# Kernel optimization log

Hardware: AMD Instinct MI355X
Metric: run time of the kernel (lower is better)

## Reference

```python
import math
import jax, jax.numpy as jnp
import numpy as np

B, T, D_MODEL, H = 8, 2048, 1024, 16
D_HEAD = D_MODEL // H


def _rel_shift(x):
    # x: (B, T, H, H) -- faithful port of the TF pad/reshape/slice trick,
    # which in this module operates on the time axis (dim 1).
    b, t, h, h2 = x.shape
    x = jnp.pad(x, ((0, 0), (1, 0), (0, 0), (0, 0)))  # (B, T+1, H, H)
    x = x.reshape(t + 1, b, h, h2)[1:]                 # drop first row
    return x.reshape(b, t, h, h2)


def setup_inputs() -> dict:
    key = jax.random.key(0)
    ks = jax.random.split(key, 16)
    s = 1.0 / math.sqrt(D_MODEL)
    return {
        "inputs": jax.random.normal(ks[0], (B, T, D_MODEL), jnp.float32),
        "pos_embedding": jax.random.normal(ks[1], (B, T, D_MODEL), jnp.float32),
        "masks": jnp.ones((B, T), dtype=bool),
        "Wq": jax.random.normal(ks[2], (D_MODEL, D_MODEL), jnp.float32) * s,
        "bq": jnp.zeros((D_MODEL,), jnp.float32),
        "Wk": jax.random.normal(ks[3], (D_MODEL, D_MODEL), jnp.float32) * s,
        "bk": jnp.zeros((D_MODEL,), jnp.float32),
        "Wv": jax.random.normal(ks[4], (D_MODEL, D_MODEL), jnp.float32) * s,
        "bv": jnp.zeros((D_MODEL,), jnp.float32),
        "Wp": jax.random.normal(ks[5], (D_MODEL, D_MODEL), jnp.float32) * s,
        "Wo": jax.random.normal(ks[6], (D_MODEL, D_MODEL), jnp.float32) * s,
        "bo": jnp.zeros((D_MODEL,), jnp.float32),
        "u_bias": jax.random.normal(ks[7], (H, D_HEAD), jnp.float32) * 0.05,
        "v_bias": jax.random.normal(ks[8], (H, D_HEAD), jnp.float32) * 0.05,
    }


def reference(inputs, pos_embedding, masks, Wq, bq, Wk, bk, Wv, bv, Wp, Wo, bo, u_bias, v_bias):
    b, t, _ = inputs.shape
    sqrt_dim = math.sqrt(D_MODEL)
    q = (inputs @ Wq + bq).reshape(b, t, H, D_HEAD)
    k = (inputs @ Wk + bk).reshape(b, t, H, D_HEAD)
    v = (inputs @ Wv + bv).reshape(b, t, H, D_HEAD)
    p = (pos_embedding @ Wp).reshape(b, t, H, D_HEAD)

    # NOTE: no (B,H,T,D) transpose in the original -> HxH scores per timestep.
    content_score = jnp.einsum("bthd,btkd->bthk", q + u_bias, k)  # (B,T,H,H)
    pos_score = jnp.einsum("bthd,btkd->bthk", q + v_bias, p)      # (B,T,H,H)
    pos_score = _rel_shift(pos_score)
    score = (content_score + pos_score) / sqrt_dim
    score = jnp.where(masks[:, :, None, None], score, jnp.float32(1e-9))
    attn = jax.nn.softmax(score, axis=-1)
    ctx = jnp.einsum("bthk,btkd->bthd", attn, v)                  # (B,T,H,D)
    ctx = ctx.transpose(0, 2, 1, 3).reshape(b, -1, D_MODEL)       # (B,T,d_model)
    return ctx @ Wo + bo
```

## Files before the change

### kernel.cpp

```cpp
#include <hip/hip_runtime.h>


typedef __attribute__((ext_vector_type(8))) short short8;
typedef __attribute__((ext_vector_type(4))) float f32x4;

__device__ __forceinline__ ushort f2bf(float f) {
    unsigned u = __float_as_uint(f);
    u += 0x7FFFu + ((u >> 16) & 1u);
    return (ushort)(u >> 16);
}
__device__ __forceinline__ float bf2f(ushort u) {
    return __uint_as_float(((unsigned)u) << 16);
}

typedef const unsigned int __attribute__((address_space(1)))* gas_t;
typedef unsigned int __attribute__((address_space(3)))* las_t;
__device__ __forceinline__ void gl_lds16(const ushort* g, ushort* l) {
    __builtin_amdgcn_global_load_lds((gas_t)g, (las_t)l, 16, 0, 0);
}

__global__ __launch_bounds__(256)
void conv_bf16_k(const float* __restrict__ in, ushort* __restrict__ out)
{
    const size_t i = ((size_t)blockIdx.x * 256 + threadIdx.x) * 8;
    float4 a = *(const float4*)(in + i);
    float4 b = *(const float4*)(in + i + 4);
    short8 o = {(short)f2bf(a.x), (short)f2bf(a.y), (short)f2bf(a.z), (short)f2bf(a.w),
                (short)f2bf(b.x), (short)f2bf(b.y), (short)f2bf(b.z), (short)f2bf(b.w)};
    *(short8*)(out + i) = o;
}

__global__ __launch_bounds__(256)
void transpose5_k(const float* __restrict__ W0, const float* __restrict__ W1,
                  const float* __restrict__ W2, const float* __restrict__ W3,
                  const float* __restrict__ W4, ushort* __restrict__ Wt)
{
    __shared__ float tile[32][33];
    const int z = blockIdx.z;
    const float* W = (z == 0) ? W0 : (z == 1) ? W1 : (z == 2) ? W2 : (z == 3) ? W3 : W4;
    ushort* dst = Wt + (size_t)z * 1024 * 1024;
    const int tx = threadIdx.x & 31;
    const int ty = threadIdx.x >> 5;
    const int n0 = blockIdx.x * 32;
    const int k0 = blockIdx.y * 32;
#pragma unroll
    for (int i = 0; i < 4; ++i)
        tile[ty + i * 8][tx] = W[(size_t)(k0 + ty + i * 8) * 1024 + n0 + tx];
    __syncthreads();
#pragma unroll
    for (int i = 0; i < 4; ++i)
        dst[(size_t)(n0 + ty + i * 8) * 1024 + k0 + tx] = f2bf(tile[tx][ty + i * 8]);
}

__global__ __launch_bounds__(256)
void bias_concat_k(const float* __restrict__ b0, const float* __restrict__ b1,
                   const float* __restrict__ b2, float* __restrict__ out)
{
    const int i = blockIdx.x * 256 + threadIdx.x;
    const int s = i >> 10;
    const int j = i & 1023;
    out[i] = (s == 0) ? b0[j] : (s == 1) ? b1[j] : b2[j];
}


#define VMC(n) asm volatile("s_waitcnt vmcnt(" #n ")" ::: "memory")
#define KDIM 1024

template<int HAS_BIAS, int OUT_BF16>
__global__ __launch_bounds__(512, 2)
void gemm9_k(const ushort* __restrict__ A, const ushort* __restrict__ Bt,
             const float* __restrict__ bias, void* __restrict__ Cv,
             int N)
{
    __shared__ ushort As[3 * 4096];
    __shared__ ushort Bs[3 * 8192];
    const int tid = threadIdx.x;
    const int l = tid & 63;
    const int w = tid >> 6;
    const int wr = w >> 2;
    const int wc = w & 3;

    const int gx = gridDim.x;
    const int lin = blockIdx.y * gx + blockIdx.x;
    const int xcd = lin & 7;
    const int idx = lin >> 3;
    const int hb = gridDim.y >> 3;
    const int sxc = gx >> 2;
    const int g4 = idx >> 4;
    const int li = idx & 15;
    const int bx = (g4 % sxc) * 4 + (li & 3);
    const int by = xcd * hb + (g4 / sxc) * 4 + (li >> 2);
    const int bm = by * 128;
    const int bn = bx * 256;

    const int srow = tid >> 2;
    const int scol = ((tid & 3) ^ ((tid >> 3) & 3)) * 8;
    const ushort* Ag  = A  + (size_t)(bm + srow) * KDIM + scol;
    const ushort* Bg  = Bt + (size_t)(bn + srow) * KDIM + scol;
    const ushort* Bg2 = Bg + (size_t)128 * KDIM;
    const int lw = w * 512;

    const int lr = l & 15;
    const int fb = (((l >> 4) ^ ((l >> 1) & 3)) * 8);
    const int laneA = (wr * 64 + lr) * 32 + fb;
    const int laneB = (wc * 64 + lr) * 32 + fb;

    f32x4 acc[4][4];
#pragma unroll
    for (int i = 0; i < 4; ++i)
#pragma unroll
        for (int n = 0; n < 4; ++n)
            acc[i][n] = (f32x4){0.f, 0.f, 0.f, 0.f};

    short8 fa[2][4], fbv[2][4];

#define STAGE9(tt, rg) do { \
    ushort* ha = As + (rg) * 4096 + lw; \
    ushort* hbp = Bs + (rg) * 8192 + lw; \
    const size_t ko = (size_t)(tt) * 32; \
    gl_lds16(Ag + ko, ha); \
    gl_lds16(Bg + ko, hbp); \
    gl_lds16(Bg2 + ko, hbp + 4096); \
} while (0)

    STAGE9(0, 0);
    STAGE9(1, 1);
    VMC(3);
    __builtin_amdgcn_s_barrier();
    __builtin_amdgcn_sched_barrier(0);

#pragma unroll
    for (int t = 0; t < 32; ++t) {
        const int cur = t % 3;
        const int stg = (t + 2) % 3;
        const int pb = t & 1;
        if (t + 2 < 32) STAGE9(t + 2, stg);
        const ushort* ap = As + cur * 4096 + laneA;
        const ushort* bp = Bs + cur * 8192 + laneB;
#pragma unroll
        for (int m = 0; m < 4; ++m) fa[pb][m] = *(const short8*)(ap + m * 512);
#pragma unroll
        for (int n = 0; n < 4; ++n) fbv[pb][n] = *(const short8*)(bp + n * 512);
        if (t > 0) {
            const int qb2 = (t - 1) & 1;
#pragma unroll
            for (int m = 0; m < 4; ++m)
#pragma unroll
                for (int n = 0; n < 4; ++n)
                    acc[m][n] = __builtin_amdgcn_mfma_f32_16x16x32_bf16(fa[qb2][m], fbv[qb2][n], acc[m][n], 0, 0, 0);
        }
        if (t < 30) { VMC(3); }
        else if (t == 30) { VMC(0); }
        asm volatile("s_waitcnt lgkmcnt(0)" ::: "memory");
        __builtin_amdgcn_s_barrier();
        __builtin_amdgcn_sched_barrier(0);
    }
#pragma unroll
    for (int m = 0; m < 4; ++m)
#pragma unroll
        for (int n = 0; n < 4; ++n)
            acc[m][n] = __builtin_amdgcn_mfma_f32_16x16x32_bf16(fa[1][m], fbv[1][n], acc[m][n], 0, 0, 0);
#undef STAGE9

    const int cr = (l >> 4) * 4;
    const int cc = l & 15;
    float bv[4];
#pragma unroll
    for (int n = 0; n < 4; ++n)
        bv[n] = HAS_BIAS ? bias[bn + wc * 64 + n * 16 + cc] : 0.f;
#pragma unroll
    for (int m = 0; m < 4; ++m) {
#pragma unroll
        for (int n = 0; n < 4; ++n) {
            const int col = bn + wc * 64 + n * 16 + cc;
#pragma unroll
            for (int r = 0; r < 4; ++r) {
                const int row = bm + wr * 64 + m * 16 + cr + r;
                float v = acc[m][n][r] + bv[n];
                if (OUT_BF16) ((ushort*)Cv)[(size_t)row * N + col] = f2bf(v);
                else          ((float*)Cv)[(size_t)row * N + col] = v;
            }
        }
    }
}

__global__ __launch_bounds__(256)
void attn2_k(const ushort* __restrict__ qkv, const ushort* __restrict__ pbuf,
             const float* __restrict__ ubias, const float* __restrict__ vbias,
             const int* __restrict__ masks, ushort* __restrict__ ctx)
{
    __shared__ __align__(16) float Pl[4][16 * 20];

    const int tid = threadIdx.x;
    const int w = tid >> 6;
    const int l = tid & 63;
    const int m = blockIdx.x * 4 + w;
    const int b2 = m >> 11;
    const int t2 = m & 2047;
    const int f  = m + 8;
    const int bs = f / 2049;
    const int ts = f - bs * 2049;
    const bool haspos = (ts != 0);
    const int mp = bs * 2048 + ts - 1;

    const int lr = l & 15;
    const int g  = l >> 4;
    const int ko = g * 8;

    const ushort* qb = qkv + (size_t)m * 3072;

    short8 quf[2], kf[2], qvf[2], pf[2];
#pragma unroll
    for (int c = 0; c < 2; ++c) {
        const int off = lr * 64 + c * 32 + ko;
        short8 q = *(const short8*)(qb + off);
        kf[c]    = *(const short8*)(qb + 1024 + off);
        float4 u0 = *(const float4*)(ubias + off);
        float4 u1 = *(const float4*)(ubias + off + 4);
        quf[c] = (short8){
            (short)f2bf(bf2f((ushort)q[0]) + u0.x), (short)f2bf(bf2f((ushort)q[1]) + u0.y),
            (short)f2bf(bf2f((ushort)q[2]) + u0.z), (short)f2bf(bf2f((ushort)q[3]) + u0.w),
            (short)f2bf(bf2f((ushort)q[4]) + u1.x), (short)f2bf(bf2f((ushort)q[5]) + u1.y),
            (short)f2bf(bf2f((ushort)q[6]) + u1.z), (short)f2bf(bf2f((ushort)q[7]) + u1.w)};
    }
    if (haspos) {
        const ushort* qmp = qkv + (size_t)mp * 3072;
        const ushort* pp  = pbuf + (size_t)mp * 1024;
#pragma unroll
        for (int c = 0; c < 2; ++c) {
            const int off = lr * 64 + c * 32 + ko;
            short8 q = *(const short8*)(qmp + off);
            pf[c]    = *(const short8*)(pp + off);
            float4 v0 = *(const float4*)(vbias + off);
            float4 v1 = *(const float4*)(vbias + off + 4);
            qvf[c] = (short8){
                (short)f2bf(bf2f((ushort)q[0]) + v0.x), (short)f2bf(bf2f((ushort)q[1]) + v0.y),
                (short)f2bf(bf2f((ushort)q[2]) + v0.z), (short)f2bf(bf2f((ushort)q[3]) + v0.w),
                (short)f2bf(bf2f((ushort)q[4]) + v1.x), (short)f2bf(bf2f((ushort)q[5]) + v1.y),
                (short)f2bf(bf2f((ushort)q[6]) + v1.z), (short)f2bf(bf2f((ushort)q[7]) + v1.w)};
        }
    }

    f32x4 s = (f32x4){0.f, 0.f, 0.f, 0.f};
    s = __builtin_amdgcn_mfma_f32_16x16x32_bf16(quf[0], kf[0], s, 0, 0, 0);
    s = __builtin_amdgcn_mfma_f32_16x16x32_bf16(quf[1], kf[1], s, 0, 0, 0);
    if (haspos) {
        s = __builtin_amdgcn_mfma_f32_16x16x32_bf16(qvf[0], pf[0], s, 0, 0, 0);
        s = __builtin_amdgcn_mfma_f32_16x16x32_bf16(qvf[1], pf[1], s, 0, 0, 0);
    }

    const bool mk = (masks[m] != 0);
    float sc[4];
#pragma unroll
    for (int r = 0; r < 4; ++r)
        sc[r] = mk ? s[r] * 0.03125f : 1e-9f;

    float mx[4], ex[4], sm[4];
#pragma unroll
    for (int r = 0; r < 4; ++r) {
        mx[r] = sc[r];
#pragma unroll
        for (int o = 8; o; o >>= 1) mx[r] = fmaxf(mx[r], __shfl_xor(mx[r], o, 64));
        ex[r] = __expf(sc[r] - mx[r]);
        sm[r] = ex[r];
#pragma unroll
        for (int o = 8; o; o >>= 1) sm[r] += __shfl_xor(sm[r], o, 64);
    }

    float* pw = Pl[w];
#pragma unroll
    for (int r = 0; r < 4; ++r)
        pw[(g * 4 + r) * 20 + lr] = ex[r] / sm[r];

    short8 pa;
    if (g < 2) {
        float4 p0 = *(const float4*)(pw + lr * 20 + g * 8);
        float4 p1 = *(const float4*)(pw + lr * 20 + g * 8 + 4);
        pa = (short8){(short)f2bf(p0.x), (short)f2bf(p0.y), (short)f2bf(p0.z), (short)f2bf(p0.w),
                      (short)f2bf(p1.x), (short)f2bf(p1.y), (short)f2bf(p1.z), (short)f2bf(p1.w)};
    } else {
        pa = (short8){0, 0, 0, 0, 0, 0, 0, 0};
    }

    const ushort* vb0 = qb + 2048;
    const size_t orow_base = (size_t)b2 * 2048 + (t2 >> 4);
    const int ocol_base = (t2 & 15) * 64;
#pragma unroll
    for (int n = 0; n < 4; ++n) {
        const int d0 = n * 16;
        short8 vf;
        if (g < 2) {
#pragma unroll
            for (int j = 0; j < 8; ++j)
                vf[j] = (short)vb0[(ko + j) * 64 + d0 + lr];
        } else {
            vf = (short8){0, 0, 0, 0, 0, 0, 0, 0};
        }
        f32x4 o = (f32x4){0.f, 0.f, 0.f, 0.f};
        o = __builtin_amdgcn_mfma_f32_16x16x32_bf16(pa, vf, o, 0, 0, 0);
#pragma unroll
        for (int r = 0; r < 4; ++r) {
            const int h1 = g * 4 + r;
            ctx[(orow_base + (size_t)h1 * 128) * 1024 + ocol_base + d0 + lr] = f2bf(o[r]);
        }
    }
}

extern "C" void kernel_launch(void* const* d_in, const int* in_sizes, int n_in,
                              void* d_out, int out_size, void* d_ws, size_t ws_size,
                              hipStream_t stream)
{
    (void)in_sizes; (void)n_in; (void)out_size; (void)ws_size;
    const float* inputs = (const float*)d_in[0];
    const float* pos    = (const float*)d_in[1];
    const int*   masks  = (const int*)d_in[2];
    const float* Wq = (const float*)d_in[3];
    const float* bq = (const float*)d_in[4];
    const float* Wk = (const float*)d_in[5];
    const float* bk = (const float*)d_in[6];
    const float* Wv = (const float*)d_in[7];
    const float* bv = (const float*)d_in[8];
    const float* Wp = (const float*)d_in[9];
    const float* Wo = (const float*)d_in[10];
    const float* bo = (const float*)d_in[11];
    const float* ub = (const float*)d_in[12];
    const float* vb = (const float*)d_in[13];

    char* ws = (char*)d_ws;
    const size_t WT_SZ = (size_t)1024 * 1024 * 2;
    ushort* WT  = (ushort*)(ws);
    ushort* WqT = WT;
    ushort* WpT = (ushort*)(ws + 3 * WT_SZ);
    ushort* WoT = (ushort*)(ws + 4 * WT_SZ);
    float*  biascat = (float*)(ws + 5 * WT_SZ);
    char* bufs = ws + 5 * WT_SZ + 65536;
    const size_t S_SZ = (size_t)16384 * 1024 * 2;
    ushort* S1 = (ushort*)(bufs);
    ushort* S2 = (ushort*)(bufs + S_SZ);
    ushort* S3 = (ushort*)(bufs + 2 * S_SZ);

    dim3 blk(256);

    transpose5_k<<<dim3(32, 32, 5), blk, 0, stream>>>(Wq, Wk, Wv, Wp, Wo, WT);
    bias_concat_k<<<dim3(12), blk, 0, stream>>>(bq, bk, bv, biascat);

    conv_bf16_k<<<dim3(8192), blk, 0, stream>>>(pos, S1);
    gemm9_k<0, 1><<<dim3(4, 128), dim3(512), 0, stream>>>(S1, WpT, nullptr, S2, 1024);

    conv_bf16_k<<<dim3(8192), blk, 0, stream>>>(inputs, S1);
    gemm9_k<1, 1><<<dim3(12, 128), dim3(512), 0, stream>>>(S1, WqT, biascat, S3, 3072);

    attn2_k<<<dim3(4096), blk, 0, stream>>>(S3, S2, ub, vb, masks, S1);

    gemm9_k<1, 0><<<dim3(4, 128), dim3(512), 0, stream>>>(S1, WoT, bo, (float*)d_out, 1024);
}
```

Baseline: 275.4 us.

## Double GEMM K-tile to 64 with wider LDS swizzle and fewer barriers

The bf16 GEMM kernel now stages 64-wide K slices instead of 32, which halves the main-loop trip count and the number of block barriers. Each staged row becomes 128 bytes, so the LDS XOR swizzle widens to 8 chunks, and each stage issues six async global-to-LDS loads. The register double-buffering of fragments is removed: every iteration loads two K-halves, waits, and then runs 32 MFMAs. The triple-buffered LDS footprint grows to about 144 KB, which likely rules out two resident blocks per CU and reduces overlap of loads with compute.

```diff
diff --git a/kernel.cpp b/kernel.cpp
--- a/kernel.cpp
+++ b/kernel.cpp
@@ -68,12 +68,12 @@
 
 template<int HAS_BIAS, int OUT_BF16>
 __global__ __launch_bounds__(512, 2)
-void gemm9_k(const ushort* __restrict__ A, const ushort* __restrict__ Bt,
-             const float* __restrict__ bias, void* __restrict__ Cv,
-             int N)
-{
-    __shared__ ushort As[3 * 4096];
-    __shared__ ushort Bs[3 * 8192];
+void gemm12_k(const ushort* __restrict__ A, const ushort* __restrict__ Bt,
+              const float* __restrict__ bias, void* __restrict__ Cv,
+              int N)
+{
+    __shared__ ushort As[3 * 8192];
+    __shared__ ushort Bs[3 * 16384];
     const int tid = threadIdx.x;
     const int l = tid & 63;
     const int w = tid >> 6;
@@ -93,17 +93,17 @@
     const int bm = by * 128;
     const int bn = bx * 256;
 
-    const int srow = tid >> 2;
-    const int scol = ((tid & 3) ^ ((tid >> 3) & 3)) * 8;
-    const ushort* Ag  = A  + (size_t)(bm + srow) * KDIM + scol;
-    const ushort* Bg  = Bt + (size_t)(bn + srow) * KDIM + scol;
-    const ushort* Bg2 = Bg + (size_t)128 * KDIM;
+    const int srow = w * 8 + (l >> 3);
+    const int scol = ((l & 7) ^ ((l >> 3) & 7)) * 8;
+    const ushort* Ag = A  + (size_t)(bm + srow) * KDIM + scol;
+    const ushort* Bg = Bt + (size_t)(bn + srow) * KDIM + scol;
     const int lw = w * 512;
 
     const int lr = l & 15;
-    const int fb = (((l >> 4) ^ ((l >> 1) & 3)) * 8);
-    const int laneA = (wr * 64 + lr) * 32 + fb;
-    const int laneB = (wc * 64 + lr) * 32 + fb;
+    const int fb0 = (((l >> 4)) ^ (l & 7)) * 8;
+    const int fb1 = ((4 + (l >> 4)) ^ (l & 7)) * 8;
+    const int laneA = (wr * 64 + lr) * 64;
+    const int laneB = (wc * 64 + lr) * 64;
 
     f32x4 acc[4][4];
 #pragma unroll
@@ -112,55 +112,59 @@
         for (int n = 0; n < 4; ++n)
             acc[i][n] = (f32x4){0.f, 0.f, 0.f, 0.f};
 
-    short8 fa[2][4], fbv[2][4];
-
-#define STAGE9(tt, rg) do { \
-    ushort* ha = As + (rg) * 4096 + lw; \
-    ushort* hbp = Bs + (rg) * 8192 + lw; \
-    const size_t ko = (size_t)(tt) * 32; \
+#define STAGE12(tt, rg) do { \
+    const size_t ko = (size_t)(tt) * 64; \
+    ushort* ha = As + (rg) * 8192 + lw; \
     gl_lds16(Ag + ko, ha); \
-    gl_lds16(Bg + ko, hbp); \
-    gl_lds16(Bg2 + ko, hbp + 4096); \
+    gl_lds16(Ag + (size_t)64 * KDIM + ko, ha + 4096); \
+    ushort* hb2 = Bs + (rg) * 16384 + lw; \
+    gl_lds16(Bg + ko, hb2); \
+    gl_lds16(Bg + (size_t)64 * KDIM + ko, hb2 + 4096); \
+    gl_lds16(Bg + (size_t)128 * KDIM + ko, hb2 + 8192); \
+    gl_lds16(Bg + (size_t)192 * KDIM + ko, hb2 + 12288); \
 } while (0)
 
-    STAGE9(0, 0);
-    STAGE9(1, 1);
-    VMC(3);
+    STAGE12(0, 0);
+    STAGE12(1, 1);
+    VMC(6);
     __builtin_amdgcn_s_barrier();
     __builtin_amdgcn_sched_barrier(0);
 
 #pragma unroll
-    for (int t = 0; t < 32; ++t) {
+    for (int t = 0; t < 16; ++t) {
         const int cur = t % 3;
         const int stg = (t + 2) % 3;
-        const int pb = t & 1;
-        if (t + 2 < 32) STAGE9(t + 2, stg);
-        const ushort* ap = As + cur * 4096 + laneA;
-        const ushort* bp = Bs + cur * 8192 + laneB;
-#pragma unroll
-        for (int m = 0; m < 4; ++m) fa[pb][m] = *(const short8*)(ap + m * 512);
-#pragma unroll
-        for (int n = 0; n < 4; ++n) fbv[pb][n] = *(const short8*)(bp + n * 512);
-        if (t > 0) {
-            const int qb2 = (t - 1) & 1;
-#pragma unroll
-            for (int m = 0; m < 4; ++m)
-#pragma unroll
-                for (int n = 0; n < 4; ++n)
-                    acc[m][n] = __builtin_amdgcn_mfma_f32_16x16x32_bf16(fa[qb2][m], fbv[qb2][n], acc[m][n], 0, 0, 0);
-        }
-        if (t < 30) { VMC(3); }
-        else if (t == 30) { VMC(0); }
+        if (t + 2 < 16) STAGE12(t + 2, stg);
+        const ushort* ap = As + cur * 8192 + laneA;
+        const ushort* bp = Bs + cur * 16384 + laneB;
+        short8 af0[4], af1[4], bf0[4], bf1[4];
+#pragma unroll
+        for (int m = 0; m < 4; ++m) {
+            af0[m] = *(const short8*)(ap + m * 1024 + fb0);
+            af1[m] = *(const short8*)(ap + m * 1024 + fb1);
+        }
+#pragma unroll
+        for (int n = 0; n < 4; ++n) {
+            bf0[n] = *(const short8*)(bp + n * 1024 + fb0);
+            bf1[n] = *(const short8*)(bp + n * 1024 + fb1);
+        }
+        if (t < 14) { VMC(6); }
+        else if (t == 14) { VMC(0); }
         asm volatile("s_waitcnt lgkmcnt(0)" ::: "memory");
         __builtin_amdgcn_s_barrier();
         __builtin_amdgcn_sched_barrier(0);
-    }
-#pragma unroll
-    for (int m = 0; m < 4; ++m)
-#pragma unroll
-        for (int n = 0; n < 4; ++n)
-            acc[m][n] = __builtin_amdgcn_mfma_f32_16x16x32_bf16(fa[1][m], fbv[1][n], acc[m][n], 0, 0, 0);
-#undef STAGE9
+#pragma unroll
+        for (int m = 0; m < 4; ++m)
+#pragma unroll
+            for (int n = 0; n < 4; ++n)
+                acc[m][n] = __builtin_amdgcn_mfma_f32_16x16x32_bf16(af0[m], bf0[n], acc[m][n], 0, 0, 0);
+#pragma unroll
+        for (int m = 0; m < 4; ++m)
+#pragma unroll
+            for (int n = 0; n < 4; ++n)
+                acc[m][n] = __builtin_amdgcn_mfma_f32_16x16x32_bf16(af1[m], bf1[n], acc[m][n], 0, 0, 0);
+    }
+#undef STAGE12
 
     const int cr = (l >> 4) * 4;
     const int cc = l & 15;
@@ -345,12 +349,12 @@
     bias_concat_k<<<dim3(12), blk, 0, stream>>>(bq, bk, bv, biascat);
 
     conv_bf16_k<<<dim3(8192), blk, 0, stream>>>(pos, S1);
-    gemm9_k<0, 1><<<dim3(4, 128), dim3(512), 0, stream>>>(S1, WpT, nullptr, S2, 1024);
+    gemm12_k<0, 1><<<dim3(4, 128), dim3(512), 0, stream>>>(S1, WpT, nullptr, S2, 1024);
 
     conv_bf16_k<<<dim3(8192), blk, 0, stream>>>(inputs, S1);
-    gemm9_k<1, 1><<<dim3(12, 128), dim3(512), 0, stream>>>(S1, WqT, biascat, S3, 3072);
+    gemm12_k<1, 1><<<dim3(12, 128), dim3(512), 0, stream>>>(S1, WqT, biascat, S3, 3072);
 
     attn2_k<<<dim3(4096), blk, 0, stream>>>(S3, S2, ub, vb, masks, S1);
 
-    gemm9_k<1, 0><<<dim3(4, 128), dim3(512), 0, stream>>>(S1, WoT, bo, (float*)d_out, 1024);
-}
+    gemm12_k<1, 0><<<dim3(4, 128), dim3(512), 0, stream>>>(S1, WoT, bo, (float*)d_out, 1024);
+}
```

Result: faster. 268.1 us (median of 2 runs) (-2.6%).
